# Kernel tuning notes

Measured on AMD Instinct MI355X. Metric: run time of the kernel, lower is better.

The kernel has to match this reference:

```python
import jax, jax.numpy as jnp
import numpy as np

B, N = 2, 8192
FUN, EMB = 7, 3
H = 512
HEADS = 8
DH = H // HEADS  # 64
G = 32           # slice_num
L = 4            # n_layers
OUT = 4
MLP_H = 4 * H


def _ln(x, g, b, eps=1e-5):
    m = x.mean(-1, keepdims=True)
    v = ((x - m) ** 2).mean(-1, keepdims=True)
    return (x - m) * jax.lax.rsqrt(v + eps) * g + b


def _forward(fun, emb, W_pre1, b_pre1, W_pre2, b_pre2, placeholder,
             ln1_g, ln1_b, Wfx, bfx, Wx, bx, Wslice, bslice, temp,
             Wq, Wk, Wv, Wo, bo, ln2_g, ln2_b, Wm1, bm1, Wm2, bm2,
             lnf_g, lnf_b, Wout, bout):
    b, n = fun.shape[0], fun.shape[1]
    gelu = lambda z: jax.nn.gelu(z, approximate=False)  # torch nn.GELU default (erf)
    # preprocess MLP (n_layers=0, res=False): act(pre(x)) -> post
    x = jnp.concatenate([emb, fun], axis=-1)            # [B,N,EMB+FUN]
    fx = gelu(x @ W_pre1 + b_pre1) @ W_pre2 + b_pre2    # [B,N,H]
    fx = fx + placeholder
    scale = DH ** -0.5
    for l in range(L):
        # --- physics attention (irregular mesh) ---
        h = _ln(fx, ln1_g[l], ln1_b[l])
        fx_mid = (h @ Wfx[l] + bfx[l]).reshape(b, n, HEADS, DH)  # bnhd
        x_mid = (h @ Wx[l] + bx[l]).reshape(b, n, HEADS, DH)
        logits = jnp.einsum('bnhd,dg->bnhg', x_mid, Wslice[l]) + bslice[l]
        sw = jax.nn.softmax(logits / temp[l][None, None, :, None], axis=-1)  # bnhg
        slice_mass = sw.sum(axis=1)                                   # bhg
        token = jnp.einsum('bnhd,bnhg->bhgd', fx_mid, sw)
        token = token / (slice_mass[..., None] + 1e-5)                # bhgd
        q = token @ Wq[l]
        k = token @ Wk[l]
        v = token @ Wv[l]
        attn = jax.nn.softmax(jnp.einsum('bhgd,bhkd->bhgk', q, k) * scale, axis=-1)
        out_tok = jnp.einsum('bhgk,bhkd->bhgd', attn, v)
        out = jnp.einsum('bhgd,bnhg->bnhd', out_tok, sw).reshape(b, n, H)
        fx = out @ Wo[l] + bo[l] + fx
        # --- LN + MLP (hidden = 4H) with residual ---
        h2 = _ln(fx, ln2_g[l], ln2_b[l])
        fx = gelu(h2 @ Wm1[l] + bm1[l]) @ Wm2[l] + bm2[l] + fx
    # last-layer head: LN -> Linear(out_dim)
    return _ln(fx, lnf_g, lnf_b) @ Wout + bout


def setup_inputs() -> dict:
    key = jax.random.key(0)
    ks = iter(jax.random.split(key, 64))
    nrm = lambda shape, s=0.02: jax.random.normal(next(ks), shape, jnp.float32) * s
    return dict(
        fun=jax.random.normal(next(ks), (B, N, FUN), jnp.float32),
        emb=jax.random.normal(next(ks), (B, N, EMB), jnp.float32),
        W_pre1=nrm((FUN + EMB, 2 * H)), b_pre1=jnp.zeros((2 * H,), jnp.float32),
        W_pre2=nrm((2 * H, H)), b_pre2=jnp.zeros((H,), jnp.float32),
        placeholder=nrm((H,), 1.0),
        ln1_g=jnp.ones((L, H), jnp.float32), ln1_b=jnp.zeros((L, H), jnp.float32),
        Wfx=nrm((L, H, H)), bfx=jnp.zeros((L, H), jnp.float32),
        Wx=nrm((L, H, H)), bx=jnp.zeros((L, H), jnp.float32),
        Wslice=nrm((L, DH, G), 0.1), bslice=jnp.zeros((L, G), jnp.float32),
        temp=jnp.full((L, HEADS), 0.5, jnp.float32),
        Wq=nrm((L, DH, DH)), Wk=nrm((L, DH, DH)), Wv=nrm((L, DH, DH)),
        Wo=nrm((L, H, H)), bo=jnp.zeros((L, H), jnp.float32),
        ln2_g=jnp.ones((L, H), jnp.float32), ln2_b=jnp.zeros((L, H), jnp.float32),
        Wm1=nrm((L, H, MLP_H)), bm1=jnp.zeros((L, MLP_H), jnp.float32),
        Wm2=nrm((L, MLP_H, H)), bm2=jnp.zeros((L, H), jnp.float32),
        lnf_g=jnp.ones((H,), jnp.float32), lnf_b=jnp.zeros((H,), jnp.float32),
        Wout=nrm((H, OUT)), bout=jnp.zeros((OUT,), jnp.float32),
    )


def reference(fun, emb, W_pre1, b_pre1, W_pre2, b_pre2, placeholder,
              ln1_g, ln1_b, Wfx, bfx, Wx, bx, Wslice, bslice, temp,
              Wq, Wk, Wv, Wo, bo, ln2_g, ln2_b, Wm1, bm1, Wm2, bm2,
              lnf_g, lnf_b, Wout, bout):
    return _forward(fun, emb, W_pre1, b_pre1, W_pre2, b_pre2, placeholder,
                    ln1_g, ln1_b, Wfx, bfx, Wx, bx, Wslice, bslice, temp,
                    Wq, Wk, Wv, Wo, bo, ln2_g, ln2_b, Wm1, bm1, Wm2, bm2,
                    lnf_g, lnf_b, Wout, bout)
```

## Files before the change

### kernel.cpp

```cpp
#include <hip/hip_runtime.h>
#include <hip/hip_bf16.h>
#include <cstdint>
#include <cstddef>

typedef float  f32x4  __attribute__((ext_vector_type(4)));
typedef __bf16 bf16x8 __attribute__((ext_vector_type(8)));

#define DEV __device__ __forceinline__

DEV float gelu_f(float x){ return 0.5f * x * (1.0f + erff(x * 0.70710678118654752f)); }

DEV void gl16(void* lds, const void* g){
  __builtin_amdgcn_global_load_lds((const __attribute__((address_space(1))) void*)g,
                                   (__attribute__((address_space(3))) void*)lds, 16, 0, 0);
}

static constexpr size_t OFF_FX     = 0;
static constexpr size_t OFF_H      = 33554432;
static constexpr size_t OFF_REGA   = 50331648;
static constexpr size_t OFF_COMB   = OFF_REGA;
static constexpr size_t OFF_SW     = OFF_REGA + 50331648;
static constexpr size_t OFF_MLPH   = OFF_REGA;
static constexpr size_t OFF_H1     = OFF_REGA;
static constexpr size_t OFF_OUTB   = OFF_REGA + 67108864;
static constexpr size_t OFF_PT     = OFF_OUTB + 16777216;
static constexpr size_t OFF_PTM    = OFF_PT + 2097152;
static constexpr size_t OFF_OT     = OFF_PTM + 32768;
static constexpr size_t OFF_WT     = OFF_OT + 131072;
static constexpr size_t OFF_BIAS   = OFF_WT + 23068672;

__global__ __launch_bounds__(256) void wtrans_k(const float* __restrict__ W, __bf16* __restrict__ Wt,
                                                int K, int N, size_t wstride, size_t wtstride)
{
  __shared__ float tile[64][65];
  W  += (size_t)blockIdx.z * wstride;
  Wt += (size_t)blockIdx.z * wtstride;
  int t = threadIdx.x;
  int k0 = blockIdx.x * 64, n0 = blockIdx.y * 64;
  #pragma unroll
  for (int i = 0; i < 16; i++){
    int e = t + 256*i; int kk = e >> 6, nn = e & 63;
    tile[kk][nn] = W[(size_t)(k0+kk)*N + n0+nn];
  }
  __syncthreads();
  #pragma unroll
  for (int i = 0; i < 16; i++){
    int e = t + 256*i; int nn = e >> 6, kk = e & 63;
    Wt[(size_t)(n0+nn)*K + k0+kk] = (__bf16)tile[kk][nn];
  }
}

__global__ __launch_bounds__(128) void prep_wxs_k(const float* __restrict__ Wx, const float* __restrict__ Wsl,
                                                  const float* __restrict__ bx, const float* __restrict__ bsl,
                                                  const float* __restrict__ temp,
                                                  __bf16* __restrict__ Btcat, float* __restrict__ bcat)
{
  __shared__ float wsc[64];
  int l = blockIdx.y;
  const float* Wx_l  = Wx  + (size_t)l*262144;
  const float* Wsl_l = Wsl + l*2048;
  const float* bx_l  = bx  + l*512;
  const float* bsl_l = bsl + l*32;
  __bf16* Wt_l = Btcat + (size_t)l*393216 + (size_t)512*512;
  float* blog_l = bcat + l*768 + 512;
  int hg = blockIdx.x; int h = hg >> 5, g = hg & 31;
  int t = threadIdx.x;
  if (t < 64) wsc[t] = Wsl_l[t*32 + g];
  __syncthreads();
  float invt = 1.0f / temp[l*8 + h];
  #pragma unroll
  for (int cc = 0; cc < 4; cc++){
    int c = t + cc*128;
    float a = 0.f;
    for (int d = 0; d < 64; d++) a += Wx_l[(size_t)c*512 + h*64 + d] * wsc[d];
    Wt_l[(size_t)hg*512 + c] = (__bf16)(a * invt);
  }
  if (t == 0){
    float a = 0.f;
    for (int d = 0; d < 64; d++) a += bx_l[h*64 + d] * wsc[d];
    blog_l[hg] = (a + bsl_l[g]) * invt;
  }
}

__global__ __launch_bounds__(256) void bias_setup_k(const float* __restrict__ b_pre2, const float* __restrict__ placeholder,
                                                    const float* __restrict__ bfx,
                                                    float* __restrict__ bpre2p, float* __restrict__ bcat)
{
  int i = blockIdx.x*256 + threadIdx.x;
  if (i < 512) bpre2p[i] = b_pre2[i] + placeholder[i];
  else if (i < 2560){
    int j = i - 512; int l = j >> 9, c = j & 511;
    bcat[l*768 + c] = bfx[l*512 + c];
  }
}

__global__ __launch_bounds__(256) void preproc1_k(const float* __restrict__ fun, const float* __restrict__ emb,
                                                  const float* __restrict__ W1, const float* __restrict__ b1,
                                                  __bf16* __restrict__ h1)
{
  __shared__ float w1l[10][1024];
  int t = threadIdx.x;
  for (int i = t*4; i < 10240; i += 1024) *(f32x4*)&w1l[0][i] = *(const f32x4*)&W1[i];
  __syncthreads();
  f32x4 bv = *(const f32x4*)&b1[t*4];
  int r0 = blockIdx.x * 4;
  for (int r = 0; r < 4; r++){
    int m = r0 + r;
    const float* er = emb + (size_t)m*3;
    const float* fr = fun + (size_t)m*7;
    float x[10];
    x[0]=er[0]; x[1]=er[1]; x[2]=er[2];
    #pragma unroll
    for (int c = 0; c < 7; c++) x[3+c] = fr[c];
    f32x4 acc = bv;
    #pragma unroll
    for (int c = 0; c < 10; c++){
      f32x4 wv = *(const f32x4*)&w1l[c][t*4];
      acc += x[c] * wv;
    }
    __bf16* op = h1 + (size_t)m*1024 + t*4;
    #pragma unroll
    for (int e = 0; e < 4; e++) op[e] = (__bf16)gelu_f(acc[e]);
  }
}

template<int EPI, int BN>
__global__ __launch_bounds__(512) void gemm_wide(const __bf16* __restrict__ A, const __bf16* __restrict__ Bt,
                                                 const float* __restrict__ bias, const float* __restrict__ res,
                                                 void* __restrict__ outp, void* __restrict__ outp2,
                                                 int N, int lgK)
{
  constexpr int NSUB_B = BN/16;
  constexpr int S = 16 + NSUB_B;
  constexpr int Q = S/8;
  constexpr int NJ = BN/32;
  __shared__ bf16x8 ldsAB[4][S][64];
  const int tid = threadIdx.x;
  const int w = tid >> 6, lane = tid & 63;
  const int lm = lane & 15, lq = lane >> 4;
  const int wr = w >> 1, wc = w & 1;
  const int m0 = blockIdx.x * 256, n0 = blockIdx.y * BN;
  const int niter = 1 << (lgK - 5);

  auto issue = [&](int i){
    unsigned buf = (unsigned)i & 3u;
    int kk = i << 5;
    #pragma unroll
    for (int q = 0; q < Q; q++){
      int f = w*Q + q;
      const __bf16* p = (f < 16)
        ? A  + (((size_t)(m0 + f*16 + lm)) << lgK) + kk + lq*8
        : Bt + (((size_t)(n0 + (f-16)*16 + lm)) << lgK) + kk + lq*8;
      gl16(&ldsAB[buf][f][0], p);
    }
  };

  issue(0); issue(1); issue(2);

  f32x4 acc[4][NJ] = {};

  for (int i = 0; i < niter; ++i){
    if (i + 3 < niter){
      issue(i + 3);
      if constexpr (Q == 4) __builtin_amdgcn_s_waitcnt(0x0F7C);
      else                  __builtin_amdgcn_s_waitcnt(0x0F79);
    } else if (i + 2 < niter){
      if constexpr (Q == 4) __builtin_amdgcn_s_waitcnt(0x0F78);
      else                  __builtin_amdgcn_s_waitcnt(0x0F76);
    } else if (i + 1 < niter){
      if constexpr (Q == 4) __builtin_amdgcn_s_waitcnt(0x0F74);
      else                  __builtin_amdgcn_s_waitcnt(0x0F73);
    } else {
      __builtin_amdgcn_s_waitcnt(0x0F70);
    }
    __builtin_amdgcn_s_barrier();
    const unsigned buf = (unsigned)i & 3u;
    bf16x8 af[4], bfr[NJ];
    #pragma unroll
    for (int ii = 0; ii < 4; ii++)  af[ii]  = ldsAB[buf][wr*4 + ii][lane];
    #pragma unroll
    for (int jj = 0; jj < NJ; jj++) bfr[jj] = ldsAB[buf][16 + wc*NJ + jj][lane];
    #pragma unroll
    for (int ii = 0; ii < 4; ii++)
      #pragma unroll
      for (int jj = 0; jj < NJ; jj++)
        acc[ii][jj] = __builtin_amdgcn_mfma_f32_16x16x32_bf16(af[ii], bfr[jj], acc[ii][jj], 0, 0, 0);
    __builtin_amdgcn_s_barrier();
  }

  if (EPI == 4 && blockIdx.y == 2){
    float* swp = (float*)outp2;
    #pragma unroll
    for (int ii = 0; ii < 4; ii++){
      int row0 = m0 + wr*64 + ii*16 + lq*4;
      #pragma unroll
      for (int hp = 0; hp < 4; hp++){
        int j0 = hp*2, j1 = j0 + 1;
        int h = wc*4 + hp;
        float b0 = bias[512 + wc*128 + j0*16 + lm];
        float b1 = bias[512 + wc*128 + j1*16 + lm];
        #pragma unroll
        for (int r = 0; r < 4; r++){
          int row = row0 + r;
          float v0 = acc[ii][j0][r] + b0;
          float v1 = acc[ii][j1][r] + b1;
          float mx = fmaxf(v0, v1);
          #pragma unroll
          for (int msk = 8; msk; msk >>= 1) mx = fmaxf(mx, __shfl_xor(mx, msk));
          float e0 = expf(v0 - mx), e1 = expf(v1 - mx);
          float ss = e0 + e1;
          #pragma unroll
          for (int msk = 8; msk; msk >>= 1) ss += __shfl_xor(ss, msk);
          float inv = 1.f / ss;
          int b = row >> 13, n = row & 8191;
          float* op = swp + ((size_t)(b*8 + h)*8192 + n)*32;
          op[lm]      = e0 * inv;
          op[16 + lm] = e1 * inv;
        }
      }
    }
    return;
  }

  #pragma unroll
  for (int ii = 0; ii < 4; ii++){
    int row0 = m0 + wr*64 + ii*16 + lq*4;
    #pragma unroll
    for (int jj = 0; jj < NJ; jj++){
      int col = n0 + wc*(BN/2) + jj*16 + lm;
      float bv = bias[col];
      #pragma unroll
      for (int r = 0; r < 4; r++){
        size_t idx = (size_t)(row0 + r)*N + col;
        float v = acc[ii][jj][r] + bv;
        if (EPI == 2) v += res[idx];
        if (EPI == 1) ((__bf16*)outp)[idx] = (__bf16)gelu_f(v);
        else          ((float*)outp)[idx]  = v;
      }
    }
  }
}

__global__ __launch_bounds__(256) void ln_k(const float* __restrict__ x, const float* __restrict__ g,
                                            const float* __restrict__ b, __bf16* __restrict__ out)
{
  int w = threadIdx.x >> 6, lane = threadIdx.x & 63;
  int row = blockIdx.x*4 + w;
  const float* xr = x + (size_t)row*512 + lane*8;
  float v[8];
  *(f32x4*)&v[0] = *(const f32x4*)xr;
  *(f32x4*)&v[4] = *(const f32x4*)(xr + 4);
  float s = 0.f, sq = 0.f;
  #pragma unroll
  for (int e = 0; e < 8; e++){ s += v[e]; sq += v[e]*v[e]; }
  #pragma unroll
  for (int off = 32; off; off >>= 1){ s += __shfl_xor(s, off); sq += __shfl_xor(sq, off); }
  float mean = s * (1.f/512.f);
  float var  = sq * (1.f/512.f) - mean*mean;
  float rstd = rsqrtf(var + 1e-5f);
  float gv[8], bv[8];
  *(f32x4*)&gv[0] = *(const f32x4*)(g + lane*8);
  *(f32x4*)&gv[4] = *(const f32x4*)(g + lane*8 + 4);
  *(f32x4*)&bv[0] = *(const f32x4*)(b + lane*8);
  *(f32x4*)&bv[4] = *(const f32x4*)(b + lane*8 + 4);
  __bf16* op = out + (size_t)row*512 + lane*8;
  #pragma unroll
  for (int e = 0; e < 8; e++) op[e] = (__bf16)((v[e]-mean)*rstd*gv[e] + bv[e]);
}

__global__ __launch_bounds__(256) void token_part_k(const float* __restrict__ comb, const float* __restrict__ sw,
                                                    float* __restrict__ pt, float* __restrict__ ptm)
{
  __shared__ float fxl[32][64];
  __shared__ float swl[32][32];
  int t = threadIdx.x;
  int chunk = blockIdx.x, bh = blockIdx.y;
  int b = bh >> 3, h = bh & 7;
  int d = t & 63, gg = (t >> 6) * 8;
  float acc[8] = {0,0,0,0,0,0,0,0};
  float macc = 0.f;
  for (int s = 0; s < 16; s++){
    int nbase = chunk*512 + s*32;
    __syncthreads();
    #pragma unroll
    for (int i = 0; i < 2; i++){
      int e = t + 256*i; int rv = e >> 4, c4 = e & 15;
      *(f32x4*)&fxl[rv][c4*4] = *(const f32x4*)&comb[((size_t)b*8192 + nbase + rv)*768 + h*64 + c4*4];
    }
    { int rv = t >> 3, c4 = t & 7;
      *(f32x4*)&swl[rv][c4*4] = *(const f32x4*)&sw[((size_t)bh*8192 + nbase + rv)*32 + c4*4]; }
    __syncthreads();
    for (int nn = 0; nn < 32; nn++){
      float f = fxl[nn][d];
      #pragma unroll
      for (int jj = 0; jj < 8; jj++) acc[jj] += f * swl[nn][gg+jj];
    }
    if (t < 32){ for (int nn = 0; nn < 32; nn++) macc += swl[nn][t]; }
  }
  int cb = chunk*16 + bh;
  #pragma unroll
  for (int jj = 0; jj < 8; jj++)
    pt[((size_t)cb*32 + gg + jj)*64 + d] = acc[jj];
  if (t < 32) ptm[cb*32 + t] = macc;
}

__global__ __launch_bounds__(256) void attn_k(const float* __restrict__ pt, const float* __restrict__ ptm,
                                              const float* __restrict__ Wq, const float* __restrict__ Wk,
                                              const float* __restrict__ Wv, float* __restrict__ ot)
{
  __shared__ float tok[32][64];
  __shared__ float ml[32];
  __shared__ float qq[32][65], kk2[32][65], vv[32][65];
  __shared__ float at[32][33];
  int t = threadIdx.x, bh = blockIdx.x;
  if (t < 32){
    float s = 0.f;
    for (int c = 0; c < 16; c++) s += ptm[(c*16 + bh)*32 + t];
    ml[t] = s + 1e-5f;
  }
  __syncthreads();
  #pragma unroll
  for (int i = 0; i < 8; i++){
    int e = t + 256*i; int g = e >> 6, d = e & 63;
    float s = 0.f;
    for (int c = 0; c < 16; c++) s += pt[((size_t)(c*16 + bh)*32 + g)*64 + d];
    tok[g][d] = s / ml[g];
  }
  __syncthreads();
  #pragma unroll
  for (int i = 0; i < 8; i++){
    int e = t + 256*i; int g = e >> 6, j = e & 63;
    float aq = 0.f, ak = 0.f, av = 0.f;
    for (int d = 0; d < 64; d++){
      float tv = tok[g][d];
      aq += tv * Wq[d*64 + j];
      ak += tv * Wk[d*64 + j];
      av += tv * Wv[d*64 + j];
    }
    qq[g][j] = aq; kk2[g][j] = ak; vv[g][j] = av;
  }
  __syncthreads();
  #pragma unroll
  for (int i = 0; i < 4; i++){
    int e = t + 256*i; int g = e >> 5, j2 = e & 31;
    float s2 = 0.f;
    for (int d = 0; d < 64; d++) s2 += qq[g][d] * kk2[j2][d];
    at[g][j2] = s2 * 0.125f;
  }
  __syncthreads();
  if (t < 32){
    float mx = at[t][0];
    for (int j = 1; j < 32; j++) mx = fmaxf(mx, at[t][j]);
    float ss = 0.f;
    for (int j = 0; j < 32; j++){ float e2 = expf(at[t][j]-mx); at[t][j] = e2; ss += e2; }
    float inv = 1.f / ss;
    for (int j = 0; j < 32; j++) at[t][j] *= inv;
  }
  __syncthreads();
  #pragma unroll
  for (int i = 0; i < 8; i++){
    int e = t + 256*i; int g = e >> 6, d = e & 63;
    float s3 = 0.f;
    for (int j = 0; j < 32; j++) s3 += at[g][j] * vv[j][d];
    ot[(size_t)bh*2048 + e] = s3;
  }
}

__global__ __launch_bounds__(256) void deslice_k(const float* __restrict__ ot, const float* __restrict__ sw,
                                                 __bf16* __restrict__ outb)
{
  __shared__ float otl[32][64];
  __shared__ float swl[4][33];
  int t = threadIdx.x;
  int chunk = blockIdx.x, bh = blockIdx.y;
  int b = bh >> 3, h = bh & 7;
  #pragma unroll
  for (int i = 0; i < 8; i++){
    int e = t + 256*i;
    otl[e>>6][e&63] = ot[(size_t)bh*2048 + e];
  }
  int n0 = chunk*128;
  int nsub = t >> 6, d = t & 63;
  for (int s = 0; s < 32; s++){
    __syncthreads();
    if (t < 128) swl[t>>5][t&31] = sw[((size_t)bh*8192 + n0 + s*4 + (t>>5))*32 + (t&31)];
    __syncthreads();
    float a2 = 0.f;
    #pragma unroll
    for (int g = 0; g < 32; g++) a2 += otl[g][d] * swl[nsub][g];
    int n = n0 + s*4 + nsub;
    outb[((size_t)(b*8192 + n))*512 + h*64 + d] = (__bf16)a2;
  }
}

__global__ __launch_bounds__(256) void head_k(const float* __restrict__ x, const float* __restrict__ g,
                                              const float* __restrict__ b, const float* __restrict__ Wout,
                                              const float* __restrict__ bout, float* __restrict__ out)
{
  int w = threadIdx.x >> 6, lane = threadIdx.x & 63;
  int row = blockIdx.x*4 + w;
  const float* xr = x + (size_t)row*512 + lane*8;
  float v[8];
  *(f32x4*)&v[0] = *(const f32x4*)xr;
  *(f32x4*)&v[4] = *(const f32x4*)(xr + 4);
  float s = 0.f, sq = 0.f;
  #pragma unroll
  for (int e = 0; e < 8; e++){ s += v[e]; sq += v[e]*v[e]; }
  #pragma unroll
  for (int off = 32; off; off >>= 1){ s += __shfl_xor(s, off); sq += __shfl_xor(sq, off); }
  float mean = s * (1.f/512.f);
  float rstd = rsqrtf(sq * (1.f/512.f) - mean*mean + 1e-5f);
  float o[4] = {0,0,0,0};
  #pragma unroll
  for (int e = 0; e < 8; e++){
    int c = lane*8 + e;
    float yn = (v[e]-mean)*rstd*g[c] + b[c];
    const float* wr = Wout + (size_t)c*4;
    o[0] += yn*wr[0]; o[1] += yn*wr[1]; o[2] += yn*wr[2]; o[3] += yn*wr[3];
  }
  #pragma unroll
  for (int off = 32; off; off >>= 1){
    #pragma unroll
    for (int j = 0; j < 4; j++) o[j] += __shfl_xor(o[j], off);
  }
  if (lane == 0){
    #pragma unroll
    for (int j = 0; j < 4; j++) out[(size_t)row*4 + j] = o[j] + bout[j];
  }
}

extern "C" void kernel_launch(void* const* d_in, const int* in_sizes, int n_in,
                              void* d_out, int out_size, void* d_ws, size_t ws_size,
                              hipStream_t stream)
{
  const float* fun    = (const float*)d_in[0];
  const float* emb    = (const float*)d_in[1];
  const float* W_pre1 = (const float*)d_in[2];
  const float* b_pre1 = (const float*)d_in[3];
  const float* W_pre2 = (const float*)d_in[4];
  const float* b_pre2 = (const float*)d_in[5];
  const float* placeholder = (const float*)d_in[6];
  const float* ln1_g  = (const float*)d_in[7];
  const float* ln1_b  = (const float*)d_in[8];
  const float* Wfx    = (const float*)d_in[9];
  const float* bfx    = (const float*)d_in[10];
  const float* Wx     = (const float*)d_in[11];
  const float* bx     = (const float*)d_in[12];
  const float* Wslice = (const float*)d_in[13];
  const float* bslice = (const float*)d_in[14];
  const float* temp   = (const float*)d_in[15];
  const float* Wq     = (const float*)d_in[16];
  const float* Wk     = (const float*)d_in[17];
  const float* Wv     = (const float*)d_in[18];
  const float* Wo     = (const float*)d_in[19];
  const float* bo     = (const float*)d_in[20];
  const float* ln2_g  = (const float*)d_in[21];
  const float* ln2_b  = (const float*)d_in[22];
  const float* Wm1    = (const float*)d_in[23];
  const float* bm1    = (const float*)d_in[24];
  const float* Wm2    = (const float*)d_in[25];
  const float* bm2    = (const float*)d_in[26];
  const float* lnf_g  = (const float*)d_in[27];
  const float* lnf_b  = (const float*)d_in[28];
  const float* Wout   = (const float*)d_in[29];
  const float* bout   = (const float*)d_in[30];

  char* ws = (char*)d_ws;
  float*  fx     = (float*)(ws + OFF_FX);
  __bf16* hbf    = (__bf16*)(ws + OFF_H);
  float*  comb   = (float*)(ws + OFF_COMB);
  float*  sw     = (float*)(ws + OFF_SW);
  __bf16* mlph   = (__bf16*)(ws + OFF_MLPH);
  __bf16* h1bf   = (__bf16*)(ws + OFF_H1);
  __bf16* outb   = (__bf16*)(ws + OFF_OUTB);
  float*  pt     = (float*)(ws + OFF_PT);
  float*  ptm    = (float*)(ws + OFF_PTM);
  float*  ot     = (float*)(ws + OFF_OT);
  __bf16* Wpre2t = (__bf16*)(ws + OFF_WT);
  __bf16* Btcat  = (__bf16*)(ws + OFF_WT + 1048576);
  __bf16* Wot    = (__bf16*)(ws + OFF_WT + 4194304);
  __bf16* Wm1t   = (__bf16*)(ws + OFF_WT + 6291456);
  __bf16* Wm2t   = (__bf16*)(ws + OFF_WT + 14680064);
  float*  bcat   = (float*)(ws + OFF_BIAS);
  float*  bpre2p = (float*)(ws + OFF_BIAS + 4*768*4);

  wtrans_k<<<dim3(16,8,1), 256,0,stream>>>(W_pre2, Wpre2t, 1024, 512, 0, 0);
  wtrans_k<<<dim3(8,8,4),  256,0,stream>>>(Wfx, Btcat, 512, 512, 262144, 393216);
  wtrans_k<<<dim3(8,8,4),  256,0,stream>>>(Wo,  Wot,  512, 512, 262144, 262144);
  wtrans_k<<<dim3(8,32,4), 256,0,stream>>>(Wm1, Wm1t, 512, 2048, 1048576, 1048576);
  wtrans_k<<<dim3(32,8,4), 256,0,stream>>>(Wm2, Wm2t, 2048, 512, 1048576, 1048576);
  prep_wxs_k<<<dim3(256,4),128,0,stream>>>(Wx, Wslice, bx, bslice, temp, Btcat, bcat);
  bias_setup_k<<<10,256,0,stream>>>(b_pre2, placeholder, bfx, bpre2p, bcat);

  preproc1_k<<<4096,256,0,stream>>>(fun, emb, W_pre1, b_pre1, h1bf);
  gemm_wide<0,128><<<dim3(64,4),512,0,stream>>>(h1bf, Wpre2t, bpre2p, nullptr, (void*)fx, nullptr, 512, 10);

  for (int l = 0; l < 4; l++){
    ln_k<<<4096,256,0,stream>>>(fx, ln1_g + l*512, ln1_b + l*512, hbf);
    gemm_wide<4,256><<<dim3(64,3),512,0,stream>>>(hbf, Btcat + (size_t)l*393216, bcat + l*768, nullptr, (void*)comb, (void*)sw, 768, 9);
    token_part_k<<<dim3(16,16),256,0,stream>>>(comb, sw, pt, ptm);
    attn_k<<<16,256,0,stream>>>(pt, ptm, Wq + l*4096, Wk + l*4096, Wv + l*4096, ot);
    deslice_k<<<dim3(64,16),256,0,stream>>>(ot, sw, outb);
    gemm_wide<2,128><<<dim3(64,4),512,0,stream>>>(outb, Wot + (size_t)l*262144, bo + l*512, fx, (void*)fx, nullptr, 512, 9);
    ln_k<<<4096,256,0,stream>>>(fx, ln2_g + l*512, ln2_b + l*512, hbf);
    gemm_wide<1,256><<<dim3(64,8),512,0,stream>>>(hbf, Wm1t + (size_t)l*1048576, bm1 + l*2048, nullptr, (void*)mlph, nullptr, 2048, 9);
    gemm_wide<2,128><<<dim3(64,4),512,0,stream>>>(mlph, Wm2t + (size_t)l*1048576, bm2 + l*512, fx, (void*)fx, nullptr, 512, 11);
  }

  head_k<<<4096,256,0,stream>>>(fx, lnf_g, lnf_b, Wout, bout, (float*)d_out);
}
```

Before: 1.447 ms.

## Store fx_mid as bf16, rework deslice tiling, shrink GEMM pipeline to 3 stages

The fused fx/x/slice GEMM now writes the fx_mid projection as a bf16 [N,512] buffer instead of fp32 columns of a 768-wide combined buffer. The token reduction reads bf16 and widens to float in LDS, which cuts the bytes written and read for that tensor. The deslice kernel loads a whole 128-row slice-weight tile once and gives each thread 8 rows by 4 dims, replacing 32 barrier-separated iterations with scalar stores. All gemm_wide instantiations drop from 4-deep to 3-deep LDS buffering, which lowers LDS use and may raise occupancy but hides less load latency; bf16 fx_mid also costs some accuracy.

```diff
diff --git a/kernel.cpp b/kernel.cpp
--- a/kernel.cpp
+++ b/kernel.cpp
@@ -5,6 +5,7 @@
 
 typedef float  f32x4  __attribute__((ext_vector_type(4)));
 typedef __bf16 bf16x8 __attribute__((ext_vector_type(8)));
+typedef __bf16 bf16x4 __attribute__((ext_vector_type(4)));
 
 #define DEV __device__ __forceinline__
 
@@ -18,8 +19,8 @@
 static constexpr size_t OFF_FX     = 0;
 static constexpr size_t OFF_H      = 33554432;
 static constexpr size_t OFF_REGA   = 50331648;
-static constexpr size_t OFF_COMB   = OFF_REGA;
-static constexpr size_t OFF_SW     = OFF_REGA + 50331648;
+static constexpr size_t OFF_FXMID  = OFF_REGA;
+static constexpr size_t OFF_SW     = OFF_REGA + 16777216;
 static constexpr size_t OFF_MLPH   = OFF_REGA;
 static constexpr size_t OFF_H1     = OFF_REGA;
 static constexpr size_t OFF_OUTB   = OFF_REGA + 67108864;
@@ -134,7 +135,7 @@
   constexpr int S = 16 + NSUB_B;
   constexpr int Q = S/8;
   constexpr int NJ = BN/32;
-  __shared__ bf16x8 ldsAB[4][S][64];
+  __shared__ bf16x8 ldsAB[3][S][64];
   const int tid = threadIdx.x;
   const int w = tid >> 6, lane = tid & 63;
   const int lm = lane & 15, lq = lane >> 4;
@@ -143,7 +144,7 @@
   const int niter = 1 << (lgK - 5);
 
   auto issue = [&](int i){
-    unsigned buf = (unsigned)i & 3u;
+    unsigned buf = (unsigned)i % 3u;
     int kk = i << 5;
     #pragma unroll
     for (int q = 0; q < Q; q++){
@@ -155,16 +156,13 @@
     }
   };
 
-  issue(0); issue(1); issue(2);
+  issue(0); issue(1);
 
   f32x4 acc[4][NJ] = {};
 
   for (int i = 0; i < niter; ++i){
-    if (i + 3 < niter){
-      issue(i + 3);
-      if constexpr (Q == 4) __builtin_amdgcn_s_waitcnt(0x0F7C);
-      else                  __builtin_amdgcn_s_waitcnt(0x0F79);
-    } else if (i + 2 < niter){
+    if (i + 2 < niter){
+      issue(i + 2);
       if constexpr (Q == 4) __builtin_amdgcn_s_waitcnt(0x0F78);
       else                  __builtin_amdgcn_s_waitcnt(0x0F76);
     } else if (i + 1 < niter){
@@ -174,7 +172,7 @@
       __builtin_amdgcn_s_waitcnt(0x0F70);
     }
     __builtin_amdgcn_s_barrier();
-    const unsigned buf = (unsigned)i & 3u;
+    const unsigned buf = (unsigned)i % 3u;
     bf16x8 af[4], bfr[NJ];
     #pragma unroll
     for (int ii = 0; ii < 4; ii++)  af[ii]  = ldsAB[buf][wr*4 + ii][lane];
@@ -234,8 +232,9 @@
         size_t idx = (size_t)(row0 + r)*N + col;
         float v = acc[ii][jj][r] + bv;
         if (EPI == 2) v += res[idx];
-        if (EPI == 1) ((__bf16*)outp)[idx] = (__bf16)gelu_f(v);
-        else          ((float*)outp)[idx]  = v;
+        if (EPI == 1)      ((__bf16*)outp)[idx] = (__bf16)gelu_f(v);
+        else if (EPI == 4) ((__bf16*)outp)[idx] = (__bf16)v;
+        else               ((float*)outp)[idx]  = v;
       }
     }
   }
@@ -268,7 +267,7 @@
   for (int e = 0; e < 8; e++) op[e] = (__bf16)((v[e]-mean)*rstd*gv[e] + bv[e]);
 }
 
-__global__ __launch_bounds__(256) void token_part_k(const float* __restrict__ comb, const float* __restrict__ sw,
+__global__ __launch_bounds__(256) void token_part_k(const __bf16* __restrict__ fxmid, const float* __restrict__ sw,
                                                     float* __restrict__ pt, float* __restrict__ ptm)
 {
   __shared__ float fxl[32][64];
@@ -285,7 +284,11 @@
     #pragma unroll
     for (int i = 0; i < 2; i++){
       int e = t + 256*i; int rv = e >> 4, c4 = e & 15;
-      *(f32x4*)&fxl[rv][c4*4] = *(const f32x4*)&comb[((size_t)b*8192 + nbase + rv)*768 + h*64 + c4*4];
+      bf16x4 v = *(const bf16x4*)&fxmid[((size_t)(b*8192 + nbase + rv))*512 + h*64 + c4*4];
+      fxl[rv][c4*4+0] = (float)v[0];
+      fxl[rv][c4*4+1] = (float)v[1];
+      fxl[rv][c4*4+2] = (float)v[2];
+      fxl[rv][c4*4+3] = (float)v[3];
     }
     { int rv = t >> 3, c4 = t & 7;
       *(f32x4*)&swl[rv][c4*4] = *(const f32x4*)&sw[((size_t)bh*8192 + nbase + rv)*32 + c4*4]; }
@@ -370,26 +373,43 @@
                                                  __bf16* __restrict__ outb)
 {
   __shared__ float otl[32][64];
-  __shared__ float swl[4][33];
+  __shared__ float swl[128][36];
   int t = threadIdx.x;
   int chunk = blockIdx.x, bh = blockIdx.y;
   int b = bh >> 3, h = bh & 7;
+  int n0 = chunk*128;
   #pragma unroll
   for (int i = 0; i < 8; i++){
     int e = t + 256*i;
     otl[e>>6][e&63] = ot[(size_t)bh*2048 + e];
   }
-  int n0 = chunk*128;
-  int nsub = t >> 6, d = t & 63;
-  for (int s = 0; s < 32; s++){
-    __syncthreads();
-    if (t < 128) swl[t>>5][t&31] = sw[((size_t)bh*8192 + n0 + s*4 + (t>>5))*32 + (t&31)];
-    __syncthreads();
-    float a2 = 0.f;
-    #pragma unroll
-    for (int g = 0; g < 32; g++) a2 += otl[g][d] * swl[nsub][g];
-    int n = n0 + s*4 + nsub;
-    outb[((size_t)(b*8192 + n))*512 + h*64 + d] = (__bf16)a2;
+  {
+    int r = t >> 1, half = t & 1;
+    const float* sp = sw + ((size_t)bh*8192 + n0 + r)*32 + half*16;
+    float* dp = &swl[r][half*16];
+    #pragma unroll
+    for (int q = 0; q < 4; q++) *(f32x4*)(dp + q*4) = *(const f32x4*)(sp + q*4);
+  }
+  __syncthreads();
+  const int nl = t >> 4;
+  const int d0 = (t & 15) * 4;
+  float o[8][4] = {};
+  for (int g = 0; g < 32; g++){
+    f32x4 ov = *(const f32x4*)&otl[g][d0];
+    #pragma unroll
+    for (int p = 0; p < 8; p++){
+      float s = swl[p*16 + nl][g];
+      o[p][0] += s * ov[0]; o[p][1] += s * ov[1];
+      o[p][2] += s * ov[2]; o[p][3] += s * ov[3];
+    }
+  }
+  #pragma unroll
+  for (int p = 0; p < 8; p++){
+    int n = n0 + p*16 + nl;
+    bf16x4 v;
+    v[0] = (__bf16)o[p][0]; v[1] = (__bf16)o[p][1];
+    v[2] = (__bf16)o[p][2]; v[3] = (__bf16)o[p][3];
+    *(bf16x4*)&outb[((size_t)(b*8192 + n))*512 + h*64 + d0] = v;
   }
 }
 
@@ -468,7 +488,7 @@
   char* ws = (char*)d_ws;
   float*  fx     = (float*)(ws + OFF_FX);
   __bf16* hbf    = (__bf16*)(ws + OFF_H);
-  float*  comb   = (float*)(ws + OFF_COMB);
+  __bf16* fxmid  = (__bf16*)(ws + OFF_FXMID);
   float*  sw     = (float*)(ws + OFF_SW);
   __bf16* mlph   = (__bf16*)(ws + OFF_MLPH);
   __bf16* h1bf   = (__bf16*)(ws + OFF_H1);
@@ -497,8 +517,8 @@
 
   for (int l = 0; l < 4; l++){
     ln_k<<<4096,256,0,stream>>>(fx, ln1_g + l*512, ln1_b + l*512, hbf);
-    gemm_wide<4,256><<<dim3(64,3),512,0,stream>>>(hbf, Btcat + (size_t)l*393216, bcat + l*768, nullptr, (void*)comb, (void*)sw, 768, 9);
-    token_part_k<<<dim3(16,16),256,0,stream>>>(comb, sw, pt, ptm);
+    gemm_wide<4,256><<<dim3(64,3),512,0,stream>>>(hbf, Btcat + (size_t)l*393216, bcat + l*768, nullptr, (void*)fxmid, (void*)sw, 512, 9);
+    token_part_k<<<dim3(16,16),256,0,stream>>>(fxmid, sw, pt, ptm);
     attn_k<<<16,256,0,stream>>>(pt, ptm, Wq + l*4096, Wk + l*4096, Wv + l*4096, ot);
     deslice_k<<<dim3(64,16),256,0,stream>>>(ot, sw, outb);
     gemm_wide<2,128><<<dim3(64,4),512,0,stream>>>(outb, Wot + (size_t)l*262144, bo + l*512, fx, (void*)fx, nullptr, 512, 9);
```

Result: faster. 1.341 ms (-7.3%).
